# Kernel tuning notes

Hardware: AMD Instinct MI355X
Metric: run time of the kernel (lower is better)

The kernel has to match this reference:

```python
import jax, jax.numpy as jnp
import numpy as np

B = 4          # clouds per batch
N_PER = 8192   # points per cloud
RATIO = 0.5
M = int(N_PER * RATIO)   # sampled centroids per cloud
R = 0.2        # radius
K = 64         # max_num_neighbors
C_IN = 64


def setup_inputs() -> dict:
    key = jax.random.key(0)
    k1, k2, k3, k4 = jax.random.split(key, 4)
    N = B * N_PER
    x = jax.random.normal(k1, (N, C_IN), dtype=jnp.float32)
    pos = jax.random.uniform(k2, (N, 3), dtype=jnp.float32)  # unit cube
    batch = jnp.repeat(jnp.arange(B, dtype=jnp.int32), N_PER)
    W1 = jax.random.normal(k3, (C_IN + 3, 64), dtype=jnp.float32) * (1.0 / np.sqrt(C_IN + 3))
    b1 = jnp.zeros((64,), dtype=jnp.float32)
    W2 = jax.random.normal(k4, (64, 128), dtype=jnp.float32) * (1.0 / np.sqrt(64))
    b2 = jnp.zeros((128,), dtype=jnp.float32)
    return {"x": x, "pos": pos, "batch": batch, "W1": W1, "b1": b1, "W2": W2, "b2": b2}


def _fps(posb):
    """Farthest point sampling, vectorized over clouds. posb: [B, n, 3] -> idx [B, M]."""
    d0 = jnp.sum((posb - posb[:, :1]) ** 2, axis=-1)  # dist^2 to seed point 0: [B, n]

    def step(dists, _):
        far = jnp.argmax(dists, axis=1)                              # [B]
        newp = jnp.take_along_axis(posb, far[:, None, None], axis=1)  # [B, 1, 3]
        d = jnp.sum((posb - newp) ** 2, axis=-1)                      # [B, n]
        return jnp.minimum(dists, d), far.astype(jnp.int32)

    _, rest = jax.lax.scan(step, d0, None, length=M - 1)  # rest: [M-1, B]
    return jnp.concatenate([jnp.zeros((B, 1), jnp.int32), rest.T], axis=1)  # [B, M]


def reference(x, pos, batch, W1, b1, W2, b2):
    posb = pos.reshape(B, N_PER, 3)
    xb = x.reshape(B, N_PER, C_IN)

    # --- fps ---
    idx = _fps(posb)                                         # [B, M]
    q = jnp.take_along_axis(posb, idx[:, :, None], axis=1)   # sampled centroids [B, M, 3]

    # --- radius query: K nearest neighbors within radius R (same cloud) ---
    d2 = jnp.sum((q[:, :, None, :] - posb[:, None, :, :]) ** 2, axis=-1)  # [B, M, n]
    neg = jnp.where(d2 <= R * R, -d2, -jnp.inf)
    vals, nbr = jax.lax.top_k(neg, K)                        # [B, M, K]
    valid = vals > -jnp.inf                                  # neighbor mask

    # --- PointNetConv: gather -> MLP -> masked max aggregation ---
    bidx = jnp.arange(B)[:, None, None]
    xj = xb[bidx, nbr]                                       # [B, M, K, C_IN]
    rel = posb[bidx, nbr] - q[:, :, None, :]                 # [B, M, K, 3]
    feat = jnp.concatenate([xj, rel], axis=-1)               # [B, M, K, C_IN+3]
    h = jax.nn.relu(feat @ W1 + b1)                          # [B, M, K, 64]
    h = jax.nn.relu(h @ W2 + b2)                             # [B, M, K, 128]
    h = jnp.where(valid[..., None], h, -jnp.inf)
    out = jnp.max(h, axis=2)                                 # [B, M, 128]; self-edge guarantees >=1 valid

    x_out = out.reshape(B * M, 128)
    pos_out = q.reshape(B * M, 3)
    batch_out = jnp.repeat(jnp.arange(B, dtype=batch.dtype), M)
    return x_out, pos_out, batch_out
```

## Files before the change

### kernel.cpp

```cpp
#include <hip/hip_runtime.h>
#include <stdint.h>

#define NPER 8192
#define NB 4
#define MPER 4096
#define MTOT (NB*MPER)
#define KNB 64
#define CIN 64
#define R2C 0.04f

#define POSOUT_OFF (MTOT*128)
#define BATCH_OFF  (MTOT*128 + MTOT*3)

#define PRE_OFF 2162688ull
#define PRE_BYTES 8388608ull

#define SSTR 30720

typedef float v2f __attribute__((ext_vector_type(2)));

#define FPS_T 1024
#define PTS 8
#define NCELL 512

#define OFF_XS 0
#define OFF_YS (OFF_XS + NPER*4)
#define OFF_ZS (OFF_YS + NPER*4)
#define OFF_OS (OFF_ZS + NPER*4)
#define OFF_WIN (OFF_OS + NPER*2)
#define OFF_HIST (OFF_WIN + MPER*2)
#define OFF_SCAN (OFF_HIST + NCELL*4)
#define OFF_SLOT (OFF_SCAN + NCELL*4)
#define OFF_SID0 (OFF_SLOT + 24)
#define FPS_LDS  (OFF_SID0 + 8)

template<int CTRL>
__device__ __forceinline__ unsigned dppmax(unsigned v) {
  unsigned t = (unsigned)__builtin_amdgcn_update_dpp(
      0, (int)v, CTRL, 0xf, 0xf, true);
  return v > t ? v : t;
}
__device__ __forceinline__ unsigned wave_max_u32(unsigned v) {
  v = dppmax<0x111>(v);
  v = dppmax<0x112>(v);
  v = dppmax<0x114>(v);
  v = dppmax<0x118>(v);
  v = dppmax<0x142>(v);
  v = dppmax<0x143>(v);
  return (unsigned)__builtin_amdgcn_readlane((int)v, 63);
}

__global__ __launch_bounds__(1024) void k_fps(const float* __restrict__ pos,
                                              float* __restrict__ dout)
{
#pragma clang fp contract(off)
  extern __shared__ char smem[];
  float* Xs = (float*)(smem + OFF_XS);
  float* Ys = (float*)(smem + OFF_YS);
  float* Zs = (float*)(smem + OFF_ZS);
  unsigned short* Os = (unsigned short*)(smem + OFF_OS);
  unsigned short* winb = (unsigned short*)(smem + OFF_WIN);
  unsigned* hist = (unsigned*)(smem + OFF_HIST);
  unsigned* scanb = (unsigned*)(smem + OFF_SCAN);
  unsigned long long* slot3 = (unsigned long long*)(smem + OFF_SLOT);
  unsigned* sid0p = (unsigned*)(smem + OFF_SID0);

  const int b = blockIdx.x;
  const int tid = threadIdx.x;
  const float* pb = pos + (size_t)b * NPER * 3;
  float* qo = dout + POSOUT_OFF + (size_t)b * MPER * 3;
  float* scrb = dout + (size_t)b * SSTR;
  float* gSX = scrb; float* gSY = scrb + 8192; float* gSZ = scrb + 16384;
  unsigned* gSO = (unsigned*)(scrb + 24576);
  unsigned* gCS = (unsigned*)(scrb + 28672);

  if (tid < NCELL) hist[tid] = 0u;
  if (tid == 0) { slot3[0] = 0ull; slot3[1] = 0ull; slot3[2] = 0ull; }
  __syncthreads();

  float sxv[PTS], syv[PTS], szv[PTS];
  unsigned cellv[PTS];
#pragma unroll
  for (int k = 0; k < PTS; ++k) {
    int i = k * FPS_T + tid;
    sxv[k] = pb[i*3+0]; syv[k] = pb[i*3+1]; szv[k] = pb[i*3+2];
    unsigned ix = min(7u, (unsigned)(int)(sxv[k] * 8.0f));
    unsigned iy = min(7u, (unsigned)(int)(syv[k] * 8.0f));
    unsigned iz = min(7u, (unsigned)(int)(szv[k] * 8.0f));
    cellv[k] = (ix << 6) | (iy << 3) | iz;
    atomicAdd(&hist[cellv[k]], 1u);
  }
  __syncthreads();
  if (tid < NCELL) scanb[tid] = hist[tid];
  __syncthreads();
  for (int s = 1; s < NCELL; s <<= 1) {
    unsigned v = 0u;
    if (tid >= s && tid < NCELL) v = scanb[tid - s];
    __syncthreads();
    if (tid >= s && tid < NCELL) scanb[tid] += v;
    __syncthreads();
  }
  if (tid < NCELL) {
    hist[tid] = scanb[tid] - hist[tid];
    gCS[tid+1] = scanb[tid];
  }
  if (tid == 0) gCS[0] = 0u;
  __syncthreads();
#pragma unroll
  for (int k = 0; k < PTS; ++k) {
    unsigned dst = atomicAdd(&hist[cellv[k]], 1u);
    int orig = k * FPS_T + tid;
    Xs[dst] = sxv[k]; Ys[dst] = syv[k]; Zs[dst] = szv[k];
    Os[dst] = (unsigned short)orig;
    if (orig == 0) *sid0p = dst;
  }
  __syncthreads();
  for (int e = tid; e < NPER; e += FPS_T) {
    gSX[e] = Xs[e]; gSY[e] = Ys[e]; gSZ[e] = Zs[e];
  }
  for (int e = tid; e < NPER/2; e += FPS_T)
    gSO[e] = ((const unsigned*)Os)[e];
  v2f Xp[4], Yp[4], Zp[4], Dp[4];
  unsigned RK[PTS];
  float bxlo = 3.402823466e+38f, bylo = bxlo, bzlo = bxlo;
  float bxhi = -bxlo, byhi = bxhi, bzhi = bxhi;
#pragma unroll
  for (int k = 0; k < PTS; ++k) {
    int s = tid * PTS + k;
    float xx = Xs[s], yy = Ys[s], zz = Zs[s];
    Xp[k>>1][k&1] = xx; Yp[k>>1][k&1] = yy; Zp[k>>1][k&1] = zz;
    Dp[k>>1][k&1] = 3.402823466e+38f;
    unsigned orig = Os[s];
    RK[k] = ((unsigned)(NPER - 1 - orig) << 13) | (unsigned)s;
    bxlo = fminf(bxlo, xx); bxhi = fmaxf(bxhi, xx);
    bylo = fminf(bylo, yy); byhi = fmaxf(byhi, yy);
    bzlo = fminf(bzlo, zz); bzhi = fmaxf(bzhi, zz);
  }

  unsigned long long tkey = 0ull, wkey = 0ull;
  float lmax = 3.402823466e+38f;
  unsigned sidx = *sid0p;
  for (int m = 1; m < MPER; ++m) {
    const float cx = Xs[sidx], cy = Ys[sidx], cz = Zs[sidx];
    if (tid == 0) winb[m-1] = (unsigned short)sidx;
    if (tid == 1) slot3[(m+1) % 3] = 0ull;
    float ax = fmaxf(fmaxf(__fsub_rn(bxlo, cx), __fsub_rn(cx, bxhi)), 0.0f);
    float ay = fmaxf(fmaxf(__fsub_rn(bylo, cy), __fsub_rn(cy, byhi)), 0.0f);
    float az = fmaxf(fmaxf(__fsub_rn(bzlo, cz), __fsub_rn(cz, bzhi)), 0.0f);
    float lb = ax*ax + ay*ay + az*az;
    bool upd = (lb * 0.99988f) < lmax;
    if (__ballot(upd) != 0ull) {
      if (upd) {
        v2f cx2 = {cx, cx}, cy2 = {cy, cy}, cz2 = {cz, cz};
        v2f dnp[4];
        float bd = -1.0f;
#pragma unroll
        for (int p = 0; p < 4; ++p) {
          v2f dx = Xp[p] - cx2;
          v2f dy = Yp[p] - cy2;
          v2f dz = Zp[p] - cz2;
          v2f s = (dx*dx + dy*dy) + dz*dz;
          v2f dn;
          dn.x = fminf(Dp[p].x, s.x);
          dn.y = fminf(Dp[p].y, s.y);
          Dp[p] = dn; dnp[p] = dn;
          bd = fmaxf(bd, fmaxf(dn.x, dn.y));
        }
        unsigned brk = 0u;
#pragma unroll
        for (int p = 0; p < 4; ++p) {
          brk = (dnp[p].x == bd) ? max(brk, RK[2*p])   : brk;
          brk = (dnp[p].y == bd) ? max(brk, RK[2*p+1]) : brk;
        }
        tkey = ((unsigned long long)__float_as_uint(bd) << 26) | brk;
        lmax = bd;
      }
      unsigned hi = (unsigned)(tkey >> 26);
      unsigned M = wave_max_u32(hi);
      unsigned rk = (unsigned)tkey & 0x3FFFFFFu;
      unsigned long long msk = __ballot(hi == M);
      unsigned lo;
      if (__popcll(msk) == 1) {
        int ln = (int)__builtin_ctzll(msk);
        lo = (unsigned)__builtin_amdgcn_readlane((int)rk, ln);
      } else {
        lo = wave_max_u32((hi == M) ? rk : 0u);
      }
      wkey = ((unsigned long long)M << 26) | lo;
    }
    if ((tid & 63) == 0) atomicMax(&slot3[m % 3], wkey);
    __syncthreads();
    sidx = (unsigned)(slot3[m % 3] & 0x1FFFull);
  }
  if (tid == 0) winb[MPER-1] = (unsigned short)sidx;
  __syncthreads();
  for (int e = tid; e < MPER; e += FPS_T) {
    unsigned s = winb[e];
    qo[e*3+0] = Xs[s]; qo[e*3+1] = Ys[s]; qo[e*3+2] = Zs[s];
  }
}

#define SCAP 512
__global__ __launch_bounds__(256) void k_radius(const float* __restrict__ pos,
    float* __restrict__ dout, unsigned short* __restrict__ nbr,
    int* __restrict__ cnt)
{
  __shared__ unsigned candH[4][SCAP];
  __shared__ unsigned candL[4][SCAP];
  const int wid = threadIdx.x >> 6, lane = threadIdx.x & 63;
  const int m = blockIdx.x * 4 + wid;
  const int b = m >> 12;
  const float* scrb = dout + (size_t)b * SSTR;
  const float* SX = scrb;
  const float* SY = scrb + 8192;
  const float* SZ = scrb + 16384;
  const unsigned short* SO = (const unsigned short*)(scrb + 24576);
  const unsigned* CS = (const unsigned*)(scrb + 28672);
  const float* q = dout + POSOUT_OFF + (size_t)m * 3;
  const float qx = q[0], qy = q[1], qz = q[2];
  const int ixc = min(7, (int)(qx * 8.0f));
  const int iyc = min(7, (int)(qy * 8.0f));
  const int izc = min(7, (int)(qz * 8.0f));
  const int izlo = max(izc-2, 0), izhi = min(izc+2, 7);
  unsigned s0v = 0u, s1v = 0u;
  {
    int ix = ixc + lane / 5 - 2;
    int iy = iyc + lane % 5 - 2;
    if (lane < 25 && ix >= 0 && ix < 8 && iy >= 0 && iy < 8) {
      int cb = (ix << 6) | (iy << 3);
      s0v = CS[cb + izlo];
      s1v = CS[cb + izhi + 1];
    }
  }
  unsigned cw = 0;
  for (int seg = 0; seg < 25; ++seg) {
    unsigned s0 = (unsigned)__builtin_amdgcn_readlane((int)s0v, seg);
    unsigned s1 = (unsigned)__builtin_amdgcn_readlane((int)s1v, seg);
    for (unsigned i0 = s0; i0 < s1; i0 += 64) {
      unsigned i = i0 + (unsigned)lane;
      float dx = __fsub_rn(qx, SX[i]);
      float dy = __fsub_rn(qy, SY[i]);
      float dz = __fsub_rn(qz, SZ[i]);
      float d2 = __fadd_rn(__fadd_rn(__fmul_rn(dx,dx), __fmul_rn(dy,dy)),
                           __fmul_rn(dz,dz));
      bool in = (i < s1) && (d2 <= R2C);
      unsigned long long mk = __ballot(in);
      unsigned pre = (unsigned)__popcll(mk & ((1ull << lane) - 1ull));
      if (in) {
        unsigned slot = cw + pre;
        if (slot < SCAP) {
          candH[wid][slot] = __float_as_uint(d2);
          candL[wid][slot] = (unsigned)SO[i];
        }
      }
      cw += (unsigned)__popcll(mk);
    }
  }
  if (cw > SCAP) cw = SCAP;
  for (int s = (int)cw + lane; s < SCAP; s += 64) {
    candH[wid][s] = 0xFFFFFFFFu; candL[wid][s] = 0xFFFFFFFFu;
  }
  __syncthreads();
  for (int k = 2; k <= SCAP; k <<= 1) {
    for (int j = k >> 1; j > 0; j >>= 1) {
#pragma unroll
      for (int s = 0; s < SCAP/128; ++s) {
        int t = lane + (s << 6);
        int e = ((t & ~(j-1)) << 1) | (t & (j-1));
        int p = e | j;
        unsigned aH = candH[wid][e], aL = candL[wid][e];
        unsigned cH = candH[wid][p], cL = candL[wid][p];
        bool agt = (aH > cH) || (aH == cH && aL > cL);
        bool asc = ((e & k) == 0);
        bool sw = asc ? agt : !agt && (aH != cH || aL != cL);
        if (sw) {
          candH[wid][e] = cH; candL[wid][e] = cL;
          candH[wid][p] = aH; candL[wid][p] = aL;
        }
      }
      __syncthreads();
    }
  }
  int kk = (int)cw; if (kk > KNB) kk = KNB;
  nbr[(size_t)m*KNB + lane] =
    (lane < kk) ? (unsigned short)(candL[wid][lane] & 0xFFFFu)
                : (unsigned short)0;
  if (lane == 0) {
    cnt[m] = kk;
    dout[BATCH_OFF + m] = (float)b;
  }
}

__global__ __launch_bounds__(256) void k_pre(const float* __restrict__ x,
    const float* __restrict__ W1, float* __restrict__ hp)
{
  __shared__ float Ws[64*64];
  __shared__ float Xs[64][65];
  const int t = threadIdx.x;
  const int row0 = blockIdx.x * 64;
  for (int e = t; e < 64*64; e += 256) Ws[e] = W1[e];
  for (int e = t; e < 64*64; e += 256) {
    int r = e >> 6, ch = e & 63;
    Xs[r][ch] = x[(size_t)(row0 + r) * 64 + ch];
  }
  __syncthreads();
  const int rg = t >> 4, cg = t & 15;
  const int r0 = rg << 2, c0 = cg << 2;
  float acc[4][4];
#pragma unroll
  for (int r = 0; r < 4; ++r)
#pragma unroll
    for (int c = 0; c < 4; ++c) acc[r][c] = 0.0f;
  for (int k = 0; k < 64; ++k) {
    const float4 w = *(const float4*)&Ws[(k << 6) + c0];
    const float xr[4] = {Xs[r0][k], Xs[r0+1][k], Xs[r0+2][k], Xs[r0+3][k]};
    const float wc[4] = {w.x, w.y, w.z, w.w};
#pragma unroll
    for (int r = 0; r < 4; ++r)
#pragma unroll
      for (int c = 0; c < 4; ++c)
        acc[r][c] = fmaf(xr[r], wc[c], acc[r][c]);
  }
#pragma unroll
  for (int r = 0; r < 4; ++r) {
    float4 o = {acc[r][0], acc[r][1], acc[r][2], acc[r][3]};
    *(float4*)&hp[(size_t)(row0 + r0 + r) * 64 + c0] = o;
  }
}

__global__ __launch_bounds__(128) void k_conv2(
    const float* __restrict__ hp, const float* __restrict__ pos,
    const float* __restrict__ W1, const float* __restrict__ b1,
    const float* __restrict__ W2, const float* __restrict__ b2,
    const unsigned short* __restrict__ nbr, const int* __restrict__ cntp,
    float* __restrict__ dout)
{
  __shared__ __align__(16) float bufA[68*68];
  __shared__ __align__(16) float bufB[16*136];
  __shared__ float w1p[3*64];
  __shared__ unsigned short nbr_s[64];
  __shared__ float qv[3];
  __shared__ int cnt_s;
  const int t = threadIdx.x;
  const int m = blockIdx.x;
  const int b = m >> 12;
  if (t < 64) nbr_s[t] = nbr[(size_t)m*KNB + t];
  else if (t == 64) cnt_s = cntp[m];
  else if (t >= 65 && t < 68) qv[t-65] = dout[POSOUT_OFF + (size_t)m*3 + (t-65)];
  for (int e = t; e < 192; e += 128) w1p[e] = W1[64*64 + e];
  __syncthreads();
  {
    const int h = t & 63, jj = t >> 6;
    const size_t hb = (size_t)b * NPER * 64;
    for (int j0 = 0; j0 < 64; j0 += 2) {
      int j = j0 + jj;
      int r = nbr_s[j];
      bufA[h*68 + j] = hp[hb + (size_t)r*64 + h];
    }
  }
  {
    const size_t pbb = (size_t)b * NPER * 3;
    for (int e = t; e < 192; e += 128) {
      int j = e & 63, d = e >> 6;
      int r = nbr_s[j];
      bufA[(64+d)*68 + j] = pos[pbb + (size_t)r*3 + d] - qv[d];
    }
  }
  __syncthreads();
  for (int e = t; e < 64*64; e += 128) {
    int h = e >> 6, j = e & 63;
    float v = bufA[h*68 + j];
    v = fmaf(bufA[64*68 + j], w1p[h],       v);
    v = fmaf(bufA[65*68 + j], w1p[64 + h],  v);
    v = fmaf(bufA[66*68 + j], w1p[128 + h], v);
    bufA[h*68 + j] = fmaxf(v + b1[h], 0.0f);
  }
  const int jg = t & 7, hg = t >> 3;
  const int j0 = jg << 3;
  const int c0 = hg << 3;
  v2f acc2p[8][4];
#pragma unroll
  for (int c = 0; c < 8; ++c)
#pragma unroll
    for (int jp = 0; jp < 4; ++jp) acc2p[c][jp] = (v2f){0.0f, 0.0f};
  for (int hc = 0; hc < 64; hc += 16) {
    __syncthreads();
    for (int e = t; e < 16*128; e += 128) {
      int hh = e >> 7, c = e & 127;
      bufB[hh*136 + c] = W2[(size_t)(hc+hh)*128 + c];
    }
    __syncthreads();
#pragma unroll
    for (int h = 0; h < 16; ++h) {
      const float4 ja = *(const float4*)&bufA[(hc+h)*68 + j0];
      const float4 jb = *(const float4*)&bufA[(hc+h)*68 + j0 + 4];
      const float4 wa = *(const float4*)&bufB[h*136 + c0];
      const float4 wb = *(const float4*)&bufB[h*136 + c0 + 4];
      const v2f hj[4] = {{ja.x, ja.y}, {ja.z, ja.w}, {jb.x, jb.y}, {jb.z, jb.w}};
      const float wv[8] = {wa.x, wa.y, wa.z, wa.w, wb.x, wb.y, wb.z, wb.w};
#pragma unroll
      for (int c = 0; c < 8; ++c) {
        const v2f w2 = {wv[c], wv[c]};
#pragma unroll
        for (int jp = 0; jp < 4; ++jp)
          acc2p[c][jp] += w2 * hj[jp];
      }
    }
  }
  const int cntv = cnt_s;
  const float4 b2a = *(const float4*)&b2[c0];
  const float4 b2b = *(const float4*)&b2[c0 + 4];
  const float bv2[8] = {b2a.x, b2a.y, b2a.z, b2a.w, b2b.x, b2b.y, b2b.z, b2b.w};
  float best[8];
#pragma unroll
  for (int c = 0; c < 8; ++c) {
    float v = -3.402823466e+38f;
#pragma unroll
    for (int jp = 0; jp < 4; ++jp) {
      float h0v = fmaxf(acc2p[c][jp].x + bv2[c], 0.0f);
      float h1v = fmaxf(acc2p[c][jp].y + bv2[c], 0.0f);
      v = (j0 + 2*jp     < cntv) ? fmaxf(v, h0v) : v;
      v = (j0 + 2*jp + 1 < cntv) ? fmaxf(v, h1v) : v;
    }
    best[c] = v;
  }
#pragma unroll
  for (int off = 1; off < 8; off <<= 1)
#pragma unroll
    for (int c = 0; c < 8; ++c)
      best[c] = fmaxf(best[c], __shfl_xor(best[c], off));
  if (jg == 0) {
    float4 o0 = {best[0], best[1], best[2], best[3]};
    float4 o1 = {best[4], best[5], best[6], best[7]};
    *(float4*)&dout[(size_t)m*128 + c0] = o0;
    *(float4*)&dout[(size_t)m*128 + c0 + 4] = o1;
  }
}

__global__ __launch_bounds__(128) void k_conv(
    const float* __restrict__ x, const float* __restrict__ pos,
    const float* __restrict__ W1, const float* __restrict__ b1,
    const float* __restrict__ W2, const float* __restrict__ b2,
    const unsigned short* __restrict__ nbr, const int* __restrict__ cntp,
    float* __restrict__ dout)
{
  __shared__ __align__(16) float bufA[68*68];
  __shared__ __align__(16) float bufB[68*68];
  __shared__ unsigned short nbr_s[64];
  __shared__ float qv[3];
  __shared__ int cnt_s;
  const int t = threadIdx.x;
  const int m = blockIdx.x;
  const int b = m >> 12;
  if (t < 64) nbr_s[t] = nbr[(size_t)m*KNB + t];
  else if (t == 64) cnt_s = cntp[m];
  else if (t >= 65 && t < 68) qv[t-65] = dout[POSOUT_OFF + (size_t)m*3 + (t-65)];
  for (int e = t; e < 67*64; e += 128) {
    int ch = e >> 6, h = e & 63;
    bufB[ch*68 + h] = W1[e];
  }
  __syncthreads();
  {
    const int ch = t & 63, jj = t >> 6;
    const size_t xb = (size_t)b * NPER * CIN;
    for (int j0 = 0; j0 < 64; j0 += 2) {
      int j = j0 + jj;
      int r = nbr_s[j];
      bufA[ch*68 + j] = x[xb + (size_t)r*CIN + ch];
    }
  }
  {
    const size_t pbb = (size_t)b * NPER * 3;
    for (int e = t; e < 192; e += 128) {
      int j = e & 63, d = e >> 6;
      int r = nbr_s[j];
      bufA[(64+d)*68 + j] = pos[pbb + (size_t)r*3 + d] - qv[d];
    }
  }
  __syncthreads();
  const int jg = t & 7, hg = t >> 3;
  const int j0 = jg << 3;
  const int h0 = hg << 2;
  v2f accp[4][4];
#pragma unroll
  for (int hh = 0; hh < 4; ++hh)
#pragma unroll
    for (int jp = 0; jp < 4; ++jp) accp[hh][jp] = (v2f){0.0f, 0.0f};
  for (int ch = 0; ch < 67; ++ch) {
    const float4 fa = *(const float4*)&bufA[ch*68 + j0];
    const float4 fb = *(const float4*)&bufA[ch*68 + j0 + 4];
    const float4 w  = *(const float4*)&bufB[ch*68 + h0];
    const v2f fj[4] = {{fa.x, fa.y}, {fa.z, fa.w}, {fb.x, fb.y}, {fb.z, fb.w}};
    const float ws4[4] = {w.x, w.y, w.z, w.w};
#pragma unroll
    for (int hh = 0; hh < 4; ++hh) {
      const v2f wv2 = {ws4[hh], ws4[hh]};
#pragma unroll
      for (int jp = 0; jp < 4; ++jp)
        accp[hh][jp] += wv2 * fj[jp];
    }
  }
  __syncthreads();
  {
    const float4 bb = *(const float4*)&b1[h0];
    const float bv[4] = {bb.x, bb.y, bb.z, bb.w};
#pragma unroll
    for (int hh = 0; hh < 4; ++hh) {
      float4 o0, o1;
      o0.x = fmaxf(accp[hh][0].x + bv[hh], 0.0f);
      o0.y = fmaxf(accp[hh][0].y + bv[hh], 0.0f);
      o0.z = fmaxf(accp[hh][1].x + bv[hh], 0.0f);
      o0.w = fmaxf(accp[hh][1].y + bv[hh], 0.0f);
      o1.x = fmaxf(accp[hh][2].x + bv[hh], 0.0f);
      o1.y = fmaxf(accp[hh][2].y + bv[hh], 0.0f);
      o1.z = fmaxf(accp[hh][3].x + bv[hh], 0.0f);
      o1.w = fmaxf(accp[hh][3].y + bv[hh], 0.0f);
      *(float4*)&bufA[(h0+hh)*68 + j0] = o0;
      *(float4*)&bufA[(h0+hh)*68 + j0 + 4] = o1;
    }
  }
  const int c0 = hg << 3;
  v2f acc2p[8][4];
#pragma unroll
  for (int c = 0; c < 8; ++c)
#pragma unroll
    for (int jp = 0; jp < 4; ++jp) acc2p[c][jp] = (v2f){0.0f, 0.0f};
  for (int hc = 0; hc < 64; hc += 16) {
    __syncthreads();
    for (int e = t; e < 16*128; e += 128) {
      int hh = e >> 7, c = e & 127;
      bufB[hh*136 + c] = W2[(size_t)(hc+hh)*128 + c];
    }
    __syncthreads();
#pragma unroll
    for (int h = 0; h < 16; ++h) {
      const float4 ja = *(const float4*)&bufA[(hc+h)*68 + j0];
      const float4 jb = *(const float4*)&bufA[(hc+h)*68 + j0 + 4];
      const float4 wa = *(const float4*)&bufB[h*136 + c0];
      const float4 wb = *(const float4*)&bufB[h*136 + c0 + 4];
      const v2f hj[4] = {{ja.x, ja.y}, {ja.z, ja.w}, {jb.x, jb.y}, {jb.z, jb.w}};
      const float wv[8] = {wa.x, wa.y, wa.z, wa.w, wb.x, wb.y, wb.z, wb.w};
#pragma unroll
      for (int c = 0; c < 8; ++c) {
        const v2f w2 = {wv[c], wv[c]};
#pragma unroll
        for (int jp = 0; jp < 4; ++jp)
          acc2p[c][jp] += w2 * hj[jp];
      }
    }
  }
  const int cntv = cnt_s;
  const float4 b2a = *(const float4*)&b2[c0];
  const float4 b2b = *(const float4*)&b2[c0 + 4];
  const float bv2[8] = {b2a.x, b2a.y, b2a.z, b2a.w, b2b.x, b2b.y, b2b.z, b2b.w};
  float best[8];
#pragma unroll
  for (int c = 0; c < 8; ++c) {
    float v = -3.402823466e+38f;
#pragma unroll
    for (int jp = 0; jp < 4; ++jp) {
      float h0v = fmaxf(acc2p[c][jp].x + bv2[c], 0.0f);
      float h1v = fmaxf(acc2p[c][jp].y + bv2[c], 0.0f);
      v = (j0 + 2*jp     < cntv) ? fmaxf(v, h0v) : v;
      v = (j0 + 2*jp + 1 < cntv) ? fmaxf(v, h1v) : v;
    }
    best[c] = v;
  }
#pragma unroll
  for (int off = 1; off < 8; off <<= 1)
#pragma unroll
    for (int c = 0; c < 8; ++c)
      best[c] = fmaxf(best[c], __shfl_xor(best[c], off));
  if (jg == 0) {
    float4 o0 = {best[0], best[1], best[2], best[3]};
    float4 o1 = {best[4], best[5], best[6], best[7]};
    *(float4*)&dout[(size_t)m*128 + c0] = o0;
    *(float4*)&dout[(size_t)m*128 + c0 + 4] = o1;
  }
}

extern "C" void kernel_launch(void* const* d_in, const int* in_sizes, int n_in,
                              void* d_out, int out_size, void* d_ws, size_t ws_size,
                              hipStream_t stream) {
  const float* x   = (const float*)d_in[0];
  const float* pos = (const float*)d_in[1];
  const float* W1  = (const float*)d_in[3];
  const float* b1  = (const float*)d_in[4];
  const float* W2  = (const float*)d_in[5];
  const float* b2  = (const float*)d_in[6];
  float* dout = (float*)d_out;
  unsigned short* nbr = (unsigned short*)d_ws;
  int* cnt = (int*)((char*)d_ws + (size_t)MTOT*KNB*2);
  float* hp = (float*)((char*)d_ws + PRE_OFF);
  const bool use_pre = (ws_size >= PRE_OFF + PRE_BYTES);

  hipLaunchKernelGGL(k_fps,    dim3(NB),     dim3(FPS_T), FPS_LDS, stream, pos, dout);
  hipLaunchKernelGGL(k_radius, dim3(MTOT/4), dim3(256),   0, stream, pos, dout, nbr, cnt);
  if (use_pre) {
    hipLaunchKernelGGL(k_pre,   dim3(NB*NPER/64), dim3(256), 0, stream, x, W1, hp);
    hipLaunchKernelGGL(k_conv2, dim3(MTOT),       dim3(128), 0, stream,
                       hp, pos, W1, b1, W2, b2, nbr, cnt, dout);
  } else {
    hipLaunchKernelGGL(k_conv,  dim3(MTOT),       dim3(128), 0, stream,
                       x, pos, W1, b1, W2, b2, nbr, cnt, dout);
  }
}
```

Baseline: 3.026 ms.

## Assign FPS points to threads in spatially compact brick order

Adds a second prefix scan over cells regrouped into 4x4x2 bricks, then builds a permutation so each thread's eight points, and each wave's points, come from one compact brick instead of a run of linear cell order. The aim is tighter per-thread and per-wave bounding boxes, so the distance-update pruning in the farthest-point-sampling loop skips more work on each iteration. It costs an extra scan, extra LDS atomics and a global permutation buffer during setup. The scratch stride grows to hold that buffer.

```diff
diff --git a/kernel.cpp b/kernel.cpp
--- a/kernel.cpp
+++ b/kernel.cpp
@@ -15,7 +15,8 @@
 #define PRE_OFF 2162688ull
 #define PRE_BYTES 8388608ull
 
-#define SSTR 30720
+#define SSTR 34816
+#define PERM_F 29200
 
 typedef float v2f __attribute__((ext_vector_type(2)));
 
@@ -32,7 +33,8 @@
 #define OFF_SCAN (OFF_HIST + NCELL*4)
 #define OFF_SLOT (OFF_SCAN + NCELL*4)
 #define OFF_SID0 (OFF_SLOT + 24)
-#define FPS_LDS  (OFF_SID0 + 8)
+#define OFF_BSC  (OFF_SID0 + 8)
+#define FPS_LDS  (OFF_BSC + NCELL*4)
 
 template<int CTRL>
 __device__ __forceinline__ unsigned dppmax(unsigned v) {
@@ -48,6 +50,13 @@
   v = dppmax<0x142>(v);
   v = dppmax<0x143>(v);
   return (unsigned)__builtin_amdgcn_readlane((int)v, 63);
+}
+
+__device__ __forceinline__ unsigned brick_key(unsigned c) {
+  unsigned ix = c >> 6, iy = (c >> 3) & 7, iz = c & 7;
+  unsigned bid = ((ix >> 2) << 3) | ((iy >> 2) << 2) | (iz >> 1);
+  unsigned lid = ((ix & 3) << 3) | ((iy & 3) << 1) | (iz & 1);
+  return (bid << 5) | lid;
 }
 
 __global__ __launch_bounds__(1024) void k_fps(const float* __restrict__ pos,
@@ -64,6 +73,7 @@
   unsigned* scanb = (unsigned*)(smem + OFF_SCAN);
   unsigned long long* slot3 = (unsigned long long*)(smem + OFF_SLOT);
   unsigned* sid0p = (unsigned*)(smem + OFF_SID0);
+  unsigned* bsc = (unsigned*)(smem + OFF_BSC);
 
   const int b = blockIdx.x;
   const int tid = threadIdx.x;
@@ -73,6 +83,7 @@
   float* gSX = scrb; float* gSY = scrb + 8192; float* gSZ = scrb + 16384;
   unsigned* gSO = (unsigned*)(scrb + 24576);
   unsigned* gCS = (unsigned*)(scrb + 28672);
+  unsigned short* gPM = (unsigned short*)(scrb + PERM_F);
 
   if (tid < NCELL) hist[tid] = 0u;
   if (tid == 0) { slot3[0] = 0ull; slot3[1] = 0ull; slot3[2] = 0ull; }
@@ -106,12 +117,38 @@
   }
   if (tid == 0) gCS[0] = 0u;
   __syncthreads();
+  if (tid < NCELL) {
+    unsigned c = (unsigned)tid;
+    unsigned cntc = scanb[c] - hist[c];
+    bsc[brick_key(c)] = cntc;
+  }
+  __syncthreads();
+  for (int s = 1; s < NCELL; s <<= 1) {
+    unsigned v = 0u;
+    if (tid >= s && tid < NCELL) v = bsc[tid - s];
+    __syncthreads();
+    if (tid >= s && tid < NCELL) bsc[tid] += v;
+    __syncthreads();
+  }
+  {
+    unsigned bst = 0u;
+    if (tid < NCELL) {
+      unsigned c = (unsigned)tid;
+      unsigned cntc = scanb[c] - hist[c];
+      bst = bsc[brick_key(c)] - cntc;
+    }
+    __syncthreads();
+    if (tid < NCELL) bsc[tid] = bst;
+  }
+  __syncthreads();
 #pragma unroll
   for (int k = 0; k < PTS; ++k) {
     unsigned dst = atomicAdd(&hist[cellv[k]], 1u);
+    unsigned p   = atomicAdd(&bsc[cellv[k]], 1u);
     int orig = k * FPS_T + tid;
     Xs[dst] = sxv[k]; Ys[dst] = syv[k]; Zs[dst] = szv[k];
     Os[dst] = (unsigned short)orig;
+    gPM[p] = (unsigned short)dst;
     if (orig == 0) *sid0p = dst;
   }
   __syncthreads();
@@ -126,7 +163,7 @@
   float bxhi = -bxlo, byhi = bxhi, bzhi = bxhi;
 #pragma unroll
   for (int k = 0; k < PTS; ++k) {
-    int s = tid * PTS + k;
+    int s = (int)gPM[tid * PTS + k];
     float xx = Xs[s], yy = Ys[s], zz = Zs[s];
     Xp[k>>1][k&1] = xx; Yp[k>>1][k&1] = yy; Zp[k>>1][k&1] = zz;
     Dp[k>>1][k&1] = 3.402823466e+38f;
```

After: 3.011 ms. About the same (-0.5%).
